# Optimization experiments

Measured on AMD Instinct MI355X. Metric: run time of the kernel, lower is better.

The kernel has to match this reference:

```python
import jax, jax.numpy as jnp
import numpy as np

def setup_inputs() -> dict:
    key = jax.random.key(0)
    ks = jax.random.split(key, 8)
    B, C, H, W = 4, 64, 64, 64
    Cr = C // 8
    s = 1.0 / np.sqrt(C)
    return {
        "x": jax.random.normal(ks[0], (B, C, H, W), jnp.float32),
        "wq": jax.random.normal(ks[1], (Cr, C), jnp.float32) * s,
        "bq": jax.random.normal(ks[2], (Cr,), jnp.float32) * 0.01,
        "wk": jax.random.normal(ks[3], (Cr, C), jnp.float32) * s,
        "bk": jax.random.normal(ks[4], (Cr,), jnp.float32) * 0.01,
        "wv": jax.random.normal(ks[5], (C, C), jnp.float32) * s,
        "bv": jax.random.normal(ks[6], (C,), jnp.float32) * 0.01,
        "gamma": jax.random.normal(ks[7], (1,), jnp.float32) * 0.1,
    }

def reference(x, wq, bq, wk, bk, wv, bv, gamma):
    B, C, H, W = x.shape
    N = H * W
    xf = x.reshape(B, C, N)  # 1x1 conv == pointwise linear over channel dim
    q = jnp.einsum("oc,bcn->bno", wq, xf) + bq[None, None, :]   # (B, N, Cr)
    k = jnp.einsum("oc,bcn->bon", wk, xf) + bk[None, :, None]   # (B, Cr, N)
    v = jnp.einsum("oc,bcn->bon", wv, xf) + bv[None, :, None]   # (B, C, N)
    attn = jnp.einsum("bno,bom->bnm", q, k)                     # (B, N, N)
    attn = jax.nn.softmax(attn, axis=-1)
    out = jnp.einsum("bcm,bnm->bcn", v, attn)                   # (B, C, N)
    out = out.reshape(B, C, H, W)
    return x + gamma[0] * out
```

## Files before the change

kernel.cpp:

```cpp
#include <hip/hip_runtime.h>

#define BB 4
#define CC 64
#define NN 4096

typedef __attribute__((ext_vector_type(8)))  short short8;
typedef __attribute__((ext_vector_type(4)))  short short4v;
typedef __attribute__((ext_vector_type(4)))  float f32x4;
typedef __attribute__((ext_vector_type(16))) float f32x16;
typedef unsigned short u16;

#define QWS_ELEMS (BB * NN * 8)

__device__ inline u16 f2bf(float x) {
    unsigned u = __float_as_uint(x);
    u = (u + 0x7fffu + ((u >> 16) & 1u)) >> 16;
    return (u16)u;
}
__device__ inline unsigned pack2rne(float a, float b) {
    return (unsigned)f2bf(a) | ((unsigned)f2bf(b) << 16);
}
__device__ inline unsigned permpack(float lo, float hi) {
    return __builtin_amdgcn_perm(__float_as_uint(hi), __float_as_uint(lo), 0x07060302);
}

__device__ inline void barrier_lgkm() {
    asm volatile("s_waitcnt lgkmcnt(0)\n\ts_barrier" ::: "memory");
}

union SH8 {
    short8 s;
    struct Halves { short4v lo, hi; } h;
    uint4 u;
};

__global__ __launch_bounds__(512) void proj_kernel(
    const float* __restrict__ x,
    const float* __restrict__ wq, const float* __restrict__ bq,
    const float* __restrict__ wk, const float* __restrict__ bk,
    const float* __restrict__ wv, const float* __restrict__ bv,
    u16* __restrict__ ws_u)
{
    u16* qws = ws_u;
    u16* kws = ws_u + QWS_ELEMS;
    u16* vws = ws_u + 2 * QWS_ELEMS;

    const int y   = blockIdx.y;
    const int pix = blockIdx.x * 512 + threadIdx.x;
    const int b   = pix >> 12;
    const int n   = pix & (NN - 1);
    const float* xb = x + ((size_t)b << 18) + n;

    if (y < 8) {
        const int v0 = y << 3;
        float av[8];
#pragma unroll
        for (int i = 0; i < 8; ++i) av[i] = bv[v0 + i];
#pragma unroll 8
        for (int c = 0; c < CC; ++c) {
            const float xv = xb[(size_t)c << 12];
#pragma unroll
            for (int i = 0; i < 8; ++i)
                av[i] += wv[(v0 + i) * CC + c] * xv;
        }
#pragma unroll
        for (int i = 0; i < 8; ++i)
            vws[(((size_t)((b << 6) + v0 + i)) << 12) + n] = f2bf(av[i]);
    } else {
        float aq[8], ak[8];
#pragma unroll
        for (int i = 0; i < 8; ++i) { aq[i] = bq[i]; ak[i] = bk[i]; }
#pragma unroll 8
        for (int c = 0; c < CC; ++c) {
            const float xv = xb[(size_t)c << 12];
#pragma unroll
            for (int i = 0; i < 8; ++i) {
                aq[i] += wq[i * CC + c] * xv;
                ak[i] += wk[i * CC + c] * xv;
            }
        }
        uint4 qp, kp;
        qp.x = pack2rne(aq[0], aq[1]); qp.y = pack2rne(aq[2], aq[3]);
        qp.z = pack2rne(aq[4], aq[5]); qp.w = pack2rne(aq[6], aq[7]);
        kp.x = pack2rne(ak[0], ak[1]); kp.y = pack2rne(ak[2], ak[3]);
        kp.z = pack2rne(ak[4], ak[5]); kp.w = pack2rne(ak[6], ak[7]);
        *(uint4*)&qws[(size_t)pix * 8] = qp;
        *(uint4*)&kws[(size_t)pix * 8] = kp;
    }
}

__global__ __launch_bounds__(256) void attn_kernel(
    const float* __restrict__ x, const float* __restrict__ gamma,
    const u16* __restrict__ ws_u, float* __restrict__ out)
{
    const u16* qws = ws_u;
    const u16* kws = ws_u + QWS_ELEMS;
    const u16* vws = ws_u + 2 * QWS_ELEMS;

    __shared__ __align__(16) char smem[33792 + 512 + 128];
    u16*   v_t    = (u16*)smem;
    float* eb     = (float*)smem;
    float* l_part = (float*)(smem + 33792);
    float* l_inv  = (float*)(smem + 33792 + 512);

    const int tid  = threadIdx.x;
    const int w    = tid >> 6;
    const int lane = tid & 63;
    const int l31  = lane & 31;
    const int lh   = lane >> 5;

    const int b  = blockIdx.y;
    const int qb = blockIdx.x << 5;
    const int bN = b << 12;

    short8 qf = {0,0,0,0,0,0,0,0};
    short8 kf = {0,0,0,0,0,0,0,0};
    if (lane < 32) {
        qf = *(const short8*)(qws + (size_t)(bN + qb + l31) * 8);
        kf = *(const short8*)(kws + (size_t)(bN + (w << 5) + l31) * 8);
    }
    short8 kn = kf;

    const int c_st = tid >> 2;
    const int oq   = (tid & 3) << 3;
    const u16* vgr = vws + (((size_t)((b << 6) + c_st)) << 12) + oq;
    const int st0  = c_st * 132 + oq;

    SH8 va[4], vb[4];
#pragma unroll
    for (int j = 0; j < 4; ++j) {
        va[j].s = *(const short8*)(vgr + 32 * j);
        *(short4v*)&v_t[st0 + 32 * j]     = va[j].h.lo;
        *(short4v*)&v_t[st0 + 32 * j + 4] = va[j].h.hi;
    }
#pragma unroll
    for (int j = 0; j < 4; ++j)
        va[j].s = *(const short8*)(vgr + 128 + 32 * j);

    const int rA = l31 * 132;
    const int rB = (32 + l31) * 132;
    const int mb = (w << 5) + (lh << 2);

    f32x16 z16, acc0, acc1;
#pragma unroll
    for (int r = 0; r < 16; ++r) { z16[r] = 0.f; acc0[r] = 0.f; acc1[r] = 0.f; }
    float ls = 0.f;

    barrier_lgkm();

    for (int it = 0; it < 32; ++it) {
        const int buf = (it & 1) * 8448;
        const int nxt = ((it + 1) & 31) << 7;
        const int nx2 = ((it + 2) & 31) << 7;

#pragma unroll
        for (int j = 0; j < 4; ++j)
            vb[j].s = *(const short8*)(vgr + nx2 + 32 * j);
        if (lane < 32)
            kn = *(const short8*)(kws + (size_t)(bN + nxt + (w << 5) + l31) * 8);

        f32x16 d = __builtin_amdgcn_mfma_f32_32x32x16_bf16(kf, qf, z16, 0, 0, 0);

        float p[16];
#pragma unroll
        for (int r = 0; r < 16; ++r) p[r] = __expf(d[r]);
        float s0 = 0.f, s1 = 0.f;
#pragma unroll
        for (int r = 0; r < 8; ++r) { s0 += p[2 * r]; s1 += p[2 * r + 1]; }
        ls += s0 + s1;

        SH8 A0, A1;
        A0.u.x = permpack(p[0],  p[1]);  A0.u.y = permpack(p[2],  p[3]);
        A0.u.z = permpack(p[4],  p[5]);  A0.u.w = permpack(p[6],  p[7]);
        A1.u.x = permpack(p[8],  p[9]);  A1.u.y = permpack(p[10], p[11]);
        A1.u.z = permpack(p[12], p[13]); A1.u.w = permpack(p[14], p[15]);

        SH8 B00, B01, B10, B11;
        B00.h.lo = *(const short4v*)&v_t[buf + rA + mb];
        B00.h.hi = *(const short4v*)&v_t[buf + rA + mb + 8];
        B01.h.lo = *(const short4v*)&v_t[buf + rB + mb];
        B01.h.hi = *(const short4v*)&v_t[buf + rB + mb + 8];
        B10.h.lo = *(const short4v*)&v_t[buf + rA + mb + 16];
        B10.h.hi = *(const short4v*)&v_t[buf + rA + mb + 24];
        B11.h.lo = *(const short4v*)&v_t[buf + rB + mb + 16];
        B11.h.hi = *(const short4v*)&v_t[buf + rB + mb + 24];

        acc0 = __builtin_amdgcn_mfma_f32_32x32x16_bf16(A0.s, B00.s, acc0, 0, 0, 0);
        acc1 = __builtin_amdgcn_mfma_f32_32x32x16_bf16(A0.s, B01.s, acc1, 0, 0, 0);
        acc0 = __builtin_amdgcn_mfma_f32_32x32x16_bf16(A1.s, B10.s, acc0, 0, 0, 0);
        acc1 = __builtin_amdgcn_mfma_f32_32x32x16_bf16(A1.s, B11.s, acc1, 0, 0, 0);

        const int ob = 8448 - buf;
#pragma unroll
        for (int j = 0; j < 4; ++j) {
            *(short4v*)&v_t[ob + st0 + 32 * j]     = va[j].h.lo;
            *(short4v*)&v_t[ob + st0 + 32 * j + 4] = va[j].h.hi;
        }
#pragma unroll
        for (int j = 0; j < 4; ++j) va[j] = vb[j];
        kf = kn;

        barrier_lgkm();
    }

    float lt = ls + __shfl_xor(ls, 32, 64);
    if (lane < 32) l_part[(w << 5) + l31] = lt;
    __syncthreads();
    if (w == 0 && lane < 32)
        l_inv[l31] = 1.0f / (l_part[l31] + l_part[32 + l31] +
                             l_part[64 + l31] + l_part[96 + l31]);

    if (w >= 2) {
        float* e0 = &eb[(((w - 2) << 1) + 0) * 1088 + lane * 17];
        float* e1 = &eb[(((w - 2) << 1) + 1) * 1088 + lane * 17];
#pragma unroll
        for (int r = 0; r < 16; ++r) { e0[r] = acc0[r]; e1[r] = acc1[r]; }
    }
    __syncthreads();
    if (w < 2) {
        const float* e0 = &eb[((w << 1) + 0) * 1088 + lane * 17];
        const float* e1 = &eb[((w << 1) + 1) * 1088 + lane * 17];
#pragma unroll
        for (int r = 0; r < 16; ++r) { acc0[r] += e0[r]; acc1[r] += e1[r]; }
    }
    __syncthreads();
    if (w == 1) {
        float* e0 = &eb[0 * 1088 + lane * 17];
        float* e1 = &eb[1 * 1088 + lane * 17];
#pragma unroll
        for (int r = 0; r < 16; ++r) { e0[r] = acc0[r]; e1[r] = acc1[r]; }
    }
    __syncthreads();
    if (w == 0) {
        const float* e0 = &eb[0 * 1088 + lane * 17];
        const float* e1 = &eb[1 * 1088 + lane * 17];
#pragma unroll
        for (int r = 0; r < 16; ++r) { acc0[r] += e0[r]; acc1[r] += e1[r]; }

        f32x4 li[4];
#pragma unroll
        for (int k = 0; k < 4; ++k)
            li[k] = *(const f32x4*)&l_inv[(k << 3) + (lh << 2)];
        const float g = gamma[0];
#pragma unroll
        for (int ch = 0; ch < 2; ++ch) {
            const int c = (ch << 5) + l31;
            const f32x16 a = ch ? acc1 : acc0;
            const size_t rowb = (((size_t)((b << 6) + c)) << 12) + qb;
#pragma unroll
            for (int k = 0; k < 4; ++k) {
                const int q0 = (k << 3) + (lh << 2);
                const float4 xv = *(const float4*)&x[rowb + q0];
                float4 o;
                o.x = xv.x + g * a[4 * k + 0] * li[k][0];
                o.y = xv.y + g * a[4 * k + 1] * li[k][1];
                o.z = xv.z + g * a[4 * k + 2] * li[k][2];
                o.w = xv.w + g * a[4 * k + 3] * li[k][3];
                *(float4*)&out[rowb + q0] = o;
            }
        }
    }
}

extern "C" void kernel_launch(void* const* d_in, const int* in_sizes, int n_in,
                              void* d_out, int out_size, void* d_ws, size_t ws_size,
                              hipStream_t stream)
{
    const float* x     = (const float*)d_in[0];
    const float* wq    = (const float*)d_in[1];
    const float* bq    = (const float*)d_in[2];
    const float* wk    = (const float*)d_in[3];
    const float* bk    = (const float*)d_in[4];
    const float* wv    = (const float*)d_in[5];
    const float* bv    = (const float*)d_in[6];
    const float* gamma = (const float*)d_in[7];
    u16*   ws  = (u16*)d_ws;
    float* out = (float*)d_out;

    hipLaunchKernelGGL(proj_kernel, dim3(BB * NN / 512, 9), dim3(512), 0, stream,
                       x, wq, bq, wk, bk, wv, bv, ws);
    hipLaunchKernelGGL(attn_kernel, dim3(NN / 32, BB), dim3(256), 0, stream,
                       x, gamma, ws, out);
}
```

Before: 111.5 us.

## Pre-tile V in projection so attention loads MFMA fragments directly from global

The projection kernel now writes V in a tiled layout, in groups of 4 pixels by 64 channels, so each wave of the attention kernel can load its MFMA B-fragments straight from global memory. This removes the shared-memory staging of V and the per-iteration block barrier. Each wave also now walks its own contiguous quarter of the keys instead of interleaving with the other waves. Q is pre-scaled by log2(e) so exp2f replaces __expf, and launch bounds request 2 blocks per SM. The trade is more scattered global and L2 traffic for V in exchange for no LDS round-trip and no synchronisation inside the loop.

```diff
diff --git a/kernel.cpp b/kernel.cpp
--- a/kernel.cpp
+++ b/kernel.cpp
@@ -3,6 +3,7 @@
 #define BB 4
 #define CC 64
 #define NN 4096
+#define LOG2E 1.44269504088896340736f
 
 typedef __attribute__((ext_vector_type(8)))  short short8;
 typedef __attribute__((ext_vector_type(4)))  short short4v;
@@ -22,10 +23,6 @@
 }
 __device__ inline unsigned permpack(float lo, float hi) {
     return __builtin_amdgcn_perm(__float_as_uint(hi), __float_as_uint(lo), 0x07060302);
-}
-
-__device__ inline void barrier_lgkm() {
-    asm volatile("s_waitcnt lgkmcnt(0)\n\ts_barrier" ::: "memory");
 }
 
 union SH8 {
@@ -63,9 +60,10 @@
             for (int i = 0; i < 8; ++i)
                 av[i] += wv[(v0 + i) * CC + c] * xv;
         }
+        u16* vdst = vws + (size_t)b * 262144 + ((n >> 2) << 8) + (n & 3);
 #pragma unroll
         for (int i = 0; i < 8; ++i)
-            vws[(((size_t)((b << 6) + v0 + i)) << 12) + n] = f2bf(av[i]);
+            vdst[(v0 + i) << 2] = f2bf(av[i]);
     } else {
         float aq[8], ak[8];
 #pragma unroll
@@ -80,8 +78,10 @@
             }
         }
         uint4 qp, kp;
-        qp.x = pack2rne(aq[0], aq[1]); qp.y = pack2rne(aq[2], aq[3]);
-        qp.z = pack2rne(aq[4], aq[5]); qp.w = pack2rne(aq[6], aq[7]);
+        qp.x = pack2rne(aq[0] * LOG2E, aq[1] * LOG2E);
+        qp.y = pack2rne(aq[2] * LOG2E, aq[3] * LOG2E);
+        qp.z = pack2rne(aq[4] * LOG2E, aq[5] * LOG2E);
+        qp.w = pack2rne(aq[6] * LOG2E, aq[7] * LOG2E);
         kp.x = pack2rne(ak[0], ak[1]); kp.y = pack2rne(ak[2], ak[3]);
         kp.z = pack2rne(ak[4], ak[5]); kp.w = pack2rne(ak[6], ak[7]);
         *(uint4*)&qws[(size_t)pix * 8] = qp;
@@ -89,7 +89,7 @@
     }
 }
 
-__global__ __launch_bounds__(256) void attn_kernel(
+__global__ __launch_bounds__(256, 2) void attn_kernel(
     const float* __restrict__ x, const float* __restrict__ gamma,
     const u16* __restrict__ ws_u, float* __restrict__ out)
 {
@@ -97,11 +97,9 @@
     const u16* kws = ws_u + QWS_ELEMS;
     const u16* vws = ws_u + 2 * QWS_ELEMS;
 
-    __shared__ __align__(16) char smem[33792 + 512 + 128];
-    u16*   v_t    = (u16*)smem;
-    float* eb     = (float*)smem;
-    float* l_part = (float*)(smem + 33792);
-    float* l_inv  = (float*)(smem + 33792 + 512);
+    __shared__ float eb[4 * 1088];
+    __shared__ float l_part[4 * 32];
+    __shared__ float l_inv[32];
 
     const int tid  = threadIdx.x;
     const int w    = tid >> 6;
@@ -114,56 +112,51 @@
     const int bN = b << 12;
 
     short8 qf = {0,0,0,0,0,0,0,0};
-    short8 kf = {0,0,0,0,0,0,0,0};
-    if (lane < 32) {
+    if (lane < 32)
         qf = *(const short8*)(qws + (size_t)(bN + qb + l31) * 8);
-        kf = *(const short8*)(kws + (size_t)(bN + (w << 5) + l31) * 8);
-    }
-    short8 kn = kf;
-
-    const int c_st = tid >> 2;
-    const int oq   = (tid & 3) << 3;
-    const u16* vgr = vws + (((size_t)((b << 6) + c_st)) << 12) + oq;
-    const int st0  = c_st * 132 + oq;
-
-    SH8 va[4], vb[4];
-#pragma unroll
-    for (int j = 0; j < 4; ++j) {
-        va[j].s = *(const short8*)(vgr + 32 * j);
-        *(short4v*)&v_t[st0 + 32 * j]     = va[j].h.lo;
-        *(short4v*)&v_t[st0 + 32 * j + 4] = va[j].h.hi;
-    }
-#pragma unroll
-    for (int j = 0; j < 4; ++j)
-        va[j].s = *(const short8*)(vgr + 128 + 32 * j);
-
-    const int rA = l31 * 132;
-    const int rB = (32 + l31) * 132;
-    const int mb = (w << 5) + (lh << 2);
+
+    const u16* kp = kws + (size_t)(bN + (w << 10) + l31) * 8;
+    short8 kf = {0,0,0,0,0,0,0,0}, kn = kf;
+    if (lane < 32) kf = *(const short8*)kp;
+    kp += 32 * 8;
+
+    const u16* vp = vws + (size_t)b * 262144 + (w << 16);
+    const int o00 = (lh << 8) + (l31 << 2);
+
+    SH8 C00, C01, C10, C11, N00, N01, N10, N11;
+    C00.h.lo = *(const short4v*)(vp + o00);
+    C00.h.hi = *(const short4v*)(vp + o00 + 512);
+    C01.h.lo = *(const short4v*)(vp + o00 + 128);
+    C01.h.hi = *(const short4v*)(vp + o00 + 640);
+    C10.h.lo = *(const short4v*)(vp + o00 + 1024);
+    C10.h.hi = *(const short4v*)(vp + o00 + 1536);
+    C11.h.lo = *(const short4v*)(vp + o00 + 1152);
+    C11.h.hi = *(const short4v*)(vp + o00 + 1664);
+    vp += 2048;
 
     f32x16 z16, acc0, acc1;
 #pragma unroll
     for (int r = 0; r < 16; ++r) { z16[r] = 0.f; acc0[r] = 0.f; acc1[r] = 0.f; }
     float ls = 0.f;
 
-    barrier_lgkm();
-
     for (int it = 0; it < 32; ++it) {
-        const int buf = (it & 1) * 8448;
-        const int nxt = ((it + 1) & 31) << 7;
-        const int nx2 = ((it + 2) & 31) << 7;
-
-#pragma unroll
-        for (int j = 0; j < 4; ++j)
-            vb[j].s = *(const short8*)(vgr + nx2 + 32 * j);
-        if (lane < 32)
-            kn = *(const short8*)(kws + (size_t)(bN + nxt + (w << 5) + l31) * 8);
+        N00.h.lo = *(const short4v*)(vp + o00);
+        N00.h.hi = *(const short4v*)(vp + o00 + 512);
+        N01.h.lo = *(const short4v*)(vp + o00 + 128);
+        N01.h.hi = *(const short4v*)(vp + o00 + 640);
+        N10.h.lo = *(const short4v*)(vp + o00 + 1024);
+        N10.h.hi = *(const short4v*)(vp + o00 + 1536);
+        N11.h.lo = *(const short4v*)(vp + o00 + 1152);
+        N11.h.hi = *(const short4v*)(vp + o00 + 1664);
+        vp += 2048;
+        if (lane < 32) kn = *(const short8*)kp;
+        kp += 32 * 8;
 
         f32x16 d = __builtin_amdgcn_mfma_f32_32x32x16_bf16(kf, qf, z16, 0, 0, 0);
 
         float p[16];
 #pragma unroll
-        for (int r = 0; r < 16; ++r) p[r] = __expf(d[r]);
+        for (int r = 0; r < 16; ++r) p[r] = exp2f(d[r]);
         float s0 = 0.f, s1 = 0.f;
 #pragma unroll
         for (int r = 0; r < 8; ++r) { s0 += p[2 * r]; s1 += p[2 * r + 1]; }
@@ -175,32 +168,13 @@
         A1.u.x = permpack(p[8],  p[9]);  A1.u.y = permpack(p[10], p[11]);
         A1.u.z = permpack(p[12], p[13]); A1.u.w = permpack(p[14], p[15]);
 
-        SH8 B00, B01, B10, B11;
-        B00.h.lo = *(const short4v*)&v_t[buf + rA + mb];
-        B00.h.hi = *(const short4v*)&v_t[buf + rA + mb + 8];
-        B01.h.lo = *(const short4v*)&v_t[buf + rB + mb];
-        B01.h.hi = *(const short4v*)&v_t[buf + rB + mb + 8];
-        B10.h.lo = *(const short4v*)&v_t[buf + rA + mb + 16];
-        B10.h.hi = *(const short4v*)&v_t[buf + rA + mb + 24];
-        B11.h.lo = *(const short4v*)&v_t[buf + rB + mb + 16];
-        B11.h.hi = *(const short4v*)&v_t[buf + rB + mb + 24];
-
-        acc0 = __builtin_amdgcn_mfma_f32_32x32x16_bf16(A0.s, B00.s, acc0, 0, 0, 0);
-        acc1 = __builtin_amdgcn_mfma_f32_32x32x16_bf16(A0.s, B01.s, acc1, 0, 0, 0);
-        acc0 = __builtin_amdgcn_mfma_f32_32x32x16_bf16(A1.s, B10.s, acc0, 0, 0, 0);
-        acc1 = __builtin_amdgcn_mfma_f32_32x32x16_bf16(A1.s, B11.s, acc1, 0, 0, 0);
-
-        const int ob = 8448 - buf;
-#pragma unroll
-        for (int j = 0; j < 4; ++j) {
-            *(short4v*)&v_t[ob + st0 + 32 * j]     = va[j].h.lo;
-            *(short4v*)&v_t[ob + st0 + 32 * j + 4] = va[j].h.hi;
-        }
-#pragma unroll
-        for (int j = 0; j < 4; ++j) va[j] = vb[j];
+        acc0 = __builtin_amdgcn_mfma_f32_32x32x16_bf16(A0.s, C00.s, acc0, 0, 0, 0);
+        acc1 = __builtin_amdgcn_mfma_f32_32x32x16_bf16(A0.s, C01.s, acc1, 0, 0, 0);
+        acc0 = __builtin_amdgcn_mfma_f32_32x32x16_bf16(A1.s, C10.s, acc0, 0, 0, 0);
+        acc1 = __builtin_amdgcn_mfma_f32_32x32x16_bf16(A1.s, C11.s, acc1, 0, 0, 0);
+
+        C00 = N00; C01 = N01; C10 = N10; C11 = N11;
         kf = kn;
-
-        barrier_lgkm();
     }
 
     float lt = ls + __shfl_xor(ls, 32, 64);
```

After: 107.8 us. -3.3%, faster.
